# Optimization experiments

Hardware: AMD Instinct MI355X
Metric: run time of the kernel (lower is better)

## Reference

```python
import jax, jax.numpy as jnp
import numpy as np

N_NODES = 50000
N_EDGES = 800000
DIM = 128
N_LAYERS = 4
EPS = 1e-5  # BatchNorm1d default eps


def setup_inputs() -> dict:
    key = jax.random.key(0)
    k_x, k_e, k_w = jax.random.split(key, 3)
    x = jax.random.normal(k_x, (N_NODES, DIM), dtype=jnp.float32)
    edge_index = jax.random.randint(k_e, (2, N_EDGES), 0, N_NODES, dtype=jnp.int32)
    # stacked per-layer params (input_dim == hidden_dim == DIM)
    Ws = jax.random.normal(k_w, (N_LAYERS, DIM, DIM), dtype=jnp.float32) * (1.0 / np.sqrt(DIM))
    bs = jnp.zeros((N_LAYERS, DIM), jnp.float32)
    gammas = jnp.ones((N_LAYERS, DIM), jnp.float32)
    betas = jnp.zeros((N_LAYERS, DIM), jnp.float32)
    return {"x": x, "edge_index": edge_index, "Ws": Ws, "bs": bs,
            "gammas": gammas, "betas": betas}


def gcn_conv(x, W, b, src, dst, n):
    # PyG GCNConv: h = X W; out = D^{-1/2}(A+I)D^{-1/2} h + b
    h = x @ W                                       # [N, D]
    deg = jnp.zeros((n,), h.dtype).at[dst].add(1.0) + 1.0  # +1 self-loop
    dis = jax.lax.rsqrt(deg)                        # deg > 0 due to self-loops
    msg = h[src] * (dis[src] * dis[dst])[:, None]   # [E, D] gather + scale
    out = jnp.zeros_like(h).at[dst].add(msg)        # scatter-add aggregate
    out = out + h * (dis * dis)[:, None]            # self-loop term, norm = 1/deg
    return out + b


def batchnorm(z, gamma, beta):
    # BatchNorm1d training-mode math: batch mean, biased variance
    mu = z.mean(axis=0)
    var = z.var(axis=0)
    return (z - mu) * jax.lax.rsqrt(var + EPS) * gamma + beta


def reference(x, edge_index, Ws, bs, gammas, betas):
    src, dst = edge_index[0], edge_index[1]
    z = x
    for i in range(N_LAYERS):
        z = gcn_conv(z, Ws[i], bs[i], src, dst, z.shape[0])
        z = jax.nn.relu(z)
        z = batchnorm(z, gammas[i], betas[i])
        # Dropout: identity (eval mode / deterministic reference)
    return z
```

## Files before the change

### kernel.cpp

```cpp
#include <hip/hip_runtime.h>

#define N_NODES 50000
#define N_EDGES 800000
#define DIM 128
#define NLAYERS 4
#define BN_EPS 1e-5f
#define SCAN_BLOCKS 196
#define WSTRIDE 136

typedef __attribute__((ext_vector_type(8))) short short8;
typedef __attribute__((ext_vector_type(4))) float f32x4;

__device__ __forceinline__ float bf2f(unsigned short u){
    union { unsigned int i; float f; } x; x.i = ((unsigned int)u) << 16; return x.f;
}
__device__ __forceinline__ unsigned short f2bf(float f){
    union { float f; unsigned int i; } x; x.f = f;
    unsigned int lsb = (x.i >> 16) & 1u;
    unsigned int r = x.i + 0x7fffu + lsb;
    return (unsigned short)(r >> 16);
}

struct P4 { int2 a, b, c, d; };

__device__ __forceinline__ P4 loadP(const int2* __restrict__ ep, int base,
                                    int sub, int lim){
    P4 p;
    int i0 = base + sub, i1 = base + 4 + sub, i2 = base + 8 + sub, i3 = base + 12 + sub;
    p.a = (i0 < lim) ? ep[i0] : make_int2(0, 0);
    p.b = (i1 < lim) ? ep[i1] : make_int2(0, 0);
    p.c = (i2 < lim) ? ep[i2] : make_int2(0, 0);
    p.d = (i3 < lim) ? ep[i3] : make_int2(0, 0);
    return p;
}


__global__ __launch_bounds__(256) void k_zero(int* __restrict__ p, int n){
    int i = blockIdx.x * 256 + threadIdx.x;
    if (i < n) p[i] = 0;
}

__global__ __launch_bounds__(256) void k_count(const int* __restrict__ dst,
                                               int* __restrict__ degcnt){
    int e = blockIdx.x * 256 + threadIdx.x;
    if (e < N_EDGES) atomicAdd(&degcnt[dst[e]], 1);
}

__global__ __launch_bounds__(256) void k_scan1(const int* __restrict__ degcnt,
                                               int* __restrict__ rowptr,
                                               int* __restrict__ bsum,
                                               float* __restrict__ dis){
    __shared__ int tmp[256];
    int t = threadIdx.x;
    int i = blockIdx.x * 256 + t;
    int v = (i < N_NODES) ? degcnt[i] : 0;
    if (i < N_NODES) dis[i] = rsqrtf((float)v + 1.0f);
    tmp[t] = v;
    __syncthreads();
    #pragma unroll
    for (int off = 1; off < 256; off <<= 1){
        int u = (t >= off) ? tmp[t - off] : 0;
        __syncthreads();
        tmp[t] += u;
        __syncthreads();
    }
    if (i < N_NODES) rowptr[i] = tmp[t] - v;
    if (t == 255) bsum[blockIdx.x] = tmp[255];
}

__global__ __launch_bounds__(256) void k_scan2(int* __restrict__ bsum){
    __shared__ int tmp[256];
    int t = threadIdx.x;
    int v = (t < SCAN_BLOCKS) ? bsum[t] : 0;
    tmp[t] = v;
    __syncthreads();
    #pragma unroll
    for (int off = 1; off < 256; off <<= 1){
        int u = (t >= off) ? tmp[t - off] : 0;
        __syncthreads();
        tmp[t] += u;
        __syncthreads();
    }
    if (t < SCAN_BLOCKS) bsum[t] = tmp[t] - v;
}

__global__ __launch_bounds__(256) void k_scan3(const int* __restrict__ bsum,
                                               int* __restrict__ rowptr,
                                               int* __restrict__ wptr){
    int i = blockIdx.x * 256 + threadIdx.x;
    if (i < N_NODES){
        int r = rowptr[i] + bsum[blockIdx.x];
        rowptr[i] = r; wptr[i] = r;
    }
    if (i == 0) rowptr[N_NODES] = N_EDGES;
}

__global__ __launch_bounds__(256) void k_fill(const int* __restrict__ src,
                                              const int* __restrict__ dst,
                                              const float* __restrict__ dis,
                                              int* __restrict__ wptr,
                                              int2* __restrict__ epair){
    int e = blockIdx.x * 256 + threadIdx.x;
    if (e < N_EDGES){
        int s = src[e], d = dst[e];
        float w = dis[s] * dis[d];
        int p = atomicAdd(&wptr[d], 1);
        int2 pr; pr.x = s; pr.y = __float_as_int(w);
        epair[p] = pr;
    }
}

template<bool HAS>
__global__ __launch_bounds__(256) void k_wprep(const float* __restrict__ W,
                                               const float* __restrict__ scsh,
                                               unsigned short* __restrict__ wthi,
                                               unsigned short* __restrict__ wtlo,
                                               float* __restrict__ bias2){
    int tid = threadIdx.x;
    if (blockIdx.x < 64){
        int idx = blockIdx.x * 256 + tid;
        int c = idx >> 7, k = idx & 127;
        float v = W[k*DIM + c];
        if (HAS) v *= scsh[k];
        unsigned short hi = f2bf(v);
        float lo = v - bf2f(hi);
        wthi[c*DIM + k] = hi;
        wtlo[c*DIM + k] = f2bf(lo);
    } else {
        __shared__ float part[256];
        int c = tid >> 1, half = tid & 1;
        float acc = 0.f;
        if (HAS){
            int k0 = half * 64;
            #pragma unroll 4
            for (int k = k0; k < k0 + 64; k++)
                acc = fmaf(scsh[DIM + k], W[k*DIM + c], acc);
        }
        part[tid] = acc;
        __syncthreads();
        if (half == 0) bias2[c] = part[2*c] + part[2*c + 1];
    }
}


template<int MODE>
__global__ __launch_bounds__(256) void k_gemm(const void* __restrict__ zraw,
                                              const unsigned short* __restrict__ wthi,
                                              const unsigned short* __restrict__ wtlo,
                                              const float* __restrict__ bias2,
                                              unsigned short* __restrict__ hb){
    __shared__ short whi[DIM * WSTRIDE];
    __shared__ short wlo[DIM * WSTRIDE];
    int tid = threadIdx.x;

    {
        const uint4* gh = (const uint4*)wthi;
        const uint4* gl = (const uint4*)wtlo;
        #pragma unroll
        for (int it = 0; it < 8; it++){
            int ch = tid + 256*it;
            int c = ch >> 4, k8 = ch & 15;
            int off = c*WSTRIDE + k8*8;
            *(uint4*)&whi[off] = gh[ch];
            *(uint4*)&wlo[off] = gl[ch];
        }
    }
    __syncthreads();

    int lane = tid & 63;
    int wv   = tid >> 6;
    int m = lane & 15;
    int q = lane >> 4;
    int row0 = blockIdx.x * 64 + wv * 16;
    int arow = row0 + m;
    bool avalid = arow < N_NODES;

    f32x4 acc[8];
    #pragma unroll
    for (int t = 0; t < 8; t++) acc[t] = (f32x4){0.f, 0.f, 0.f, 0.f};

    #pragma unroll
    for (int g = 0; g < 4; g++){
        short8 a = {0,0,0,0,0,0,0,0};
        if (avalid){
            if (MODE == 0){
                const float* xp = (const float*)zraw + (size_t)arow*DIM + g*32 + q*8;
                float4 v0 = *(const float4*)xp;
                float4 v1 = *(const float4*)(xp + 4);
                a[0] = (short)f2bf(v0.x); a[1] = (short)f2bf(v0.y);
                a[2] = (short)f2bf(v0.z); a[3] = (short)f2bf(v0.w);
                a[4] = (short)f2bf(v1.x); a[5] = (short)f2bf(v1.y);
                a[6] = (short)f2bf(v1.z); a[7] = (short)f2bf(v1.w);
            } else {
                a = *(const short8*)((const unsigned short*)zraw
                      + (size_t)g*N_NODES*32 + (size_t)arow*32 + q*8);
            }
        }
        #pragma unroll
        for (int t = 0; t < 8; t++){
            int col = t*16 + m;
            int off = col*WSTRIDE + g*32 + q*8;
            short8 bh = *(const short8*)&whi[off];
            short8 bl = *(const short8*)&wlo[off];
            acc[t] = __builtin_amdgcn_mfma_f32_16x16x32_bf16(a, bh, acc[t], 0, 0, 0);
            acc[t] = __builtin_amdgcn_mfma_f32_16x16x32_bf16(a, bl, acc[t], 0, 0, 0);
        }
    }

    #pragma unroll
    for (int t = 0; t < 8; t++){
        int colg = t*16 + m;
        float bz = bias2[colg];
        size_t base = (size_t)(t >> 1)*N_NODES*32 + (t & 1)*16 + m;
        #pragma unroll
        for (int r = 0; r < 4; r++){
            int row = row0 + q*4 + r;
            if (row < N_NODES)
                hb[base + (size_t)row*32] = f2bf(acc[t][r] + bz);
        }
    }
}

__global__ __launch_bounds__(256) void k_agg(const unsigned short* __restrict__ h,
                                             const int* __restrict__ rowptr,
                                             const int2* __restrict__ epair,
                                             const float* __restrict__ dis,
                                             const float* __restrict__ bias,
                                             unsigned short* __restrict__ out,
                                             float* __restrict__ stats){
    int lane = threadIdx.x & 63;
    int w    = threadIdx.x >> 6;
    int g    = blockIdx.x & 3;
    int sub  = lane >> 4;
    int cp   = lane & 15;
    const ushort2* hg = (const ushort2*)(h + (size_t)g * N_NODES * 32);
    ushort2* og = (ushort2*)(out + (size_t)g * N_NODES * 32);
    float b0 = bias[g*32 + 2*cp], b1 = bias[g*32 + 2*cp + 1];
    float s0 = 0.f, s1 = 0.f, q0 = 0.f, q1 = 0.f;
    int bg = blockIdx.x >> 2;
    int nstride = (gridDim.x >> 2) * 4;

    int node = bg*4 + w;
    int ne0 = 0, ne1 = 0;
    ushort2 nhv; nhv.x = 0; nhv.y = 0;
    float ndi = 0.f;
    P4 nP = {{0,0},{0,0},{0,0},{0,0}};
    if (node < N_NODES){
        ne0 = rowptr[node];
        ne1 = rowptr[node + 1];
        nhv = hg[node*16 + cp];
        ndi = dis[node];
        nP  = loadP(epair, ne0, sub, ne1);
    }

    while (node < N_NODES){
        int e0 = ne0, e1 = ne1;
        ushort2 hv = nhv;
        float di = ndi;
        P4 P = nP;

        int nnext = node + nstride;
        if (nnext < N_NODES){
            ne0 = rowptr[nnext];
            ne1 = rowptr[nnext + 1];
            nhv = hg[nnext*16 + cp];
            ndi = dis[nnext];
        } else { ne0 = 0; ne1 = 0; }

        float pa0 = 0.f, pa1 = 0.f, pb0 = 0.f, pb1 = 0.f;
        float pc0 = 0.f, pc1 = 0.f, pd0 = 0.f, pd1 = 0.f;
        if (sub == 0){
            float dii = di * di;
            pa0 = bf2f(hv.x) * dii; pa1 = bf2f(hv.y) * dii;
        }

        int e = e0;
        while (e < e1){
            int en = e + 16;
            P4 Pn = {{0,0},{0,0},{0,0},{0,0}};
            if (en < e1) Pn = loadP(epair, en, sub, e1);
            ushort2 X0 = hg[P.a.x*16 + cp];
            ushort2 X1 = hg[P.b.x*16 + cp];
            ushort2 X2 = hg[P.c.x*16 + cp];
            ushort2 X3 = hg[P.d.x*16 + cp];
            float w0 = __int_as_float(P.a.y), w1 = __int_as_float(P.b.y);
            float w2 = __int_as_float(P.c.y), w3 = __int_as_float(P.d.y);
            pa0 = fmaf(bf2f(X0.x), w0, pa0); pa1 = fmaf(bf2f(X0.y), w0, pa1);
            pb0 = fmaf(bf2f(X1.x), w1, pb0); pb1 = fmaf(bf2f(X1.y), w1, pb1);
            pc0 = fmaf(bf2f(X2.x), w2, pc0); pc1 = fmaf(bf2f(X2.y), w2, pc1);
            pd0 = fmaf(bf2f(X3.x), w3, pd0); pd1 = fmaf(bf2f(X3.y), w3, pd1);
            P = Pn;
            e = en;
        }

        float r0 = (pa0 + pb0) + (pc0 + pd0);
        float r1 = (pa1 + pb1) + (pc1 + pd1);
        r0 += __shfl_xor(r0, 16); r1 += __shfl_xor(r1, 16);
        r0 += __shfl_xor(r0, 32); r1 += __shfl_xor(r1, 32);
        if (sub == 0){
            float a0 = fmaxf(r0 + b0, 0.f);
            float a1 = fmaxf(r1 + b1, 0.f);
            ushort2 ov; ov.x = f2bf(a0); ov.y = f2bf(a1);
            og[node*16 + cp] = ov;
            s0 += a0; s1 += a1; q0 += a0*a0; q1 += a1*a1;
        }

        if (nnext < N_NODES)
            nP = loadP(epair, ne0, sub, ne1);
        node = nnext;
    }

    __shared__ float red[4][16][4];
    if (sub == 0){
        red[w][cp][0] = s0; red[w][cp][1] = s1;
        red[w][cp][2] = q0; red[w][cp][3] = q1;
    }
    __syncthreads();
    if (w == 0 && sub == 0){
        #pragma unroll
        for (int ww = 1; ww < 4; ww++){
            s0 += red[ww][cp][0]; s1 += red[ww][cp][1];
            q0 += red[ww][cp][2]; q1 += red[ww][cp][3];
        }
        int c = g*32 + 2*cp;
        atomicAdd(&stats[c],         s0);
        atomicAdd(&stats[c + 1],     s1);
        atomicAdd(&stats[DIM + c],     q0);
        atomicAdd(&stats[DIM + c + 1], q1);
    }
}

__global__ void k_bnstat(const float* __restrict__ stats,
                         const float* __restrict__ gamma,
                         const float* __restrict__ beta,
                         float* __restrict__ scsh){
    int c = threadIdx.x;
    float mu  = stats[c] * (1.0f / N_NODES);
    float var = stats[DIM + c] * (1.0f / N_NODES) - mu * mu;
    float sc  = rsqrtf(var + BN_EPS) * gamma[c];
    scsh[c] = sc;
    scsh[DIM + c] = beta[c] - mu * sc;
}

__global__ __launch_bounds__(256) void k_bn(const uint4* __restrict__ in,
                                            const float* __restrict__ scsh,
                                            float4* __restrict__ outf){
    int i = blockIdx.x * 256 + threadIdx.x;
    if (i >= N_NODES * DIM / 8) return;
    int row = i >> 4;
    int c = (i * 8) & (DIM - 1);
    int gg = c >> 5, wi = c & 31;
    uint4 raw = in[gg*(N_NODES*4) + row*4 + (wi >> 3)];
    float4 sc0 = *(const float4*)&scsh[c];
    float4 sc1 = *(const float4*)&scsh[c + 4];
    float4 sh0 = *(const float4*)&scsh[DIM + c];
    float4 sh1 = *(const float4*)&scsh[DIM + c + 4];
    unsigned int u[4] = {raw.x, raw.y, raw.z, raw.w};
    float v[8];
    #pragma unroll
    for (int j = 0; j < 4; j++){
        v[2*j]   = bf2f((unsigned short)(u[j] & 0xffff));
        v[2*j+1] = bf2f((unsigned short)(u[j] >> 16));
    }
    float4 r0, r1;
    r0.x = fmaf(v[0], sc0.x, sh0.x);
    r0.y = fmaf(v[1], sc0.y, sh0.y);
    r0.z = fmaf(v[2], sc0.z, sh0.z);
    r0.w = fmaf(v[3], sc0.w, sh0.w);
    r1.x = fmaf(v[4], sc1.x, sh1.x);
    r1.y = fmaf(v[5], sc1.y, sh1.y);
    r1.z = fmaf(v[6], sc1.z, sh1.z);
    r1.w = fmaf(v[7], sc1.w, sh1.w);
    outf[2*i]   = r0;
    outf[2*i+1] = r1;
}


extern "C" void kernel_launch(void* const* d_in, const int* in_sizes, int n_in,
                              void* d_out, int out_size, void* d_ws, size_t ws_size,
                              hipStream_t stream){
    const float* x   = (const float*)d_in[0];
    const int*   src = (const int*)d_in[1];
    const int*   dst = src + N_EDGES;
    const float* Ws  = (const float*)d_in[2];
    const float* bs  = (const float*)d_in[3];
    const float* gs  = (const float*)d_in[4];
    const float* be  = (const float*)d_in[5];

    char* w = (char*)d_ws;
    int*   degcnt = (int*)(w);
    float* stats  = (float*)(w + 200000);
    float* scsh   = (float*)(w + 204096);
    float* dis    = (float*)(w + 208192);
    int*   rowptr = (int*)(w + 408192);
    int*   wptr   = (int*)(w + 608208);
    int*   bsum   = (int*)(w + 808208);
    float* bias2  = (float*)(w + 809232);
    unsigned short* wthi = (unsigned short*)(w + 809744);
    unsigned short* wtlo = (unsigned short*)(w + 842512);
    int2*  epair  = (int2*)(w + 875280);
    unsigned short* bufA = (unsigned short*)(w + 7275280);
    unsigned short* hb   = (unsigned short*)(w + 20075280);

    k_zero<<<(51024 + 255)/256, 256, 0, stream>>>(degcnt, 51024);
    k_count<<<3125, 256, 0, stream>>>(dst, degcnt);
    k_scan1<<<SCAN_BLOCKS, 256, 0, stream>>>(degcnt, rowptr, bsum, dis);
    k_scan2<<<1, 256, 0, stream>>>(bsum);
    k_scan3<<<SCAN_BLOCKS, 256, 0, stream>>>(bsum, rowptr, wptr);
    k_fill<<<3125, 256, 0, stream>>>(src, dst, dis, wptr, epair);

    for (int L = 0; L < NLAYERS; L++){
        const float* Wl = Ws + L*DIM*DIM;
        if (L == 0){
            k_wprep<false><<<65, 256, 0, stream>>>(Wl, nullptr, wthi, wtlo, bias2);
            k_gemm<0><<<(N_NODES + 63)/64, 256, 0, stream>>>(x, wthi, wtlo,
                                                             bias2, hb);
        } else {
            k_wprep<true><<<65, 256, 0, stream>>>(Wl, scsh + (L-1)*256,
                                                  wthi, wtlo, bias2);
            k_gemm<1><<<(N_NODES + 63)/64, 256, 0, stream>>>(bufA, wthi, wtlo,
                                                             bias2, hb);
        }
        k_agg<<<2048, 256, 0, stream>>>(hb, rowptr, epair, dis, bs + L*DIM,
                                        bufA, stats + L*256);
        k_bnstat<<<1, 128, 0, stream>>>(stats + L*256, gs + L*DIM, be + L*DIM,
                                        scsh + L*256);
    }
    k_bn<<<3125, 256, 0, stream>>>((const uint4*)bufA, scsh + 3*256,
                                   (float4*)d_out);
}
```

Measured before the change: 593.7 us.

## Fold BN stats into consumers, halve GEMM LDS footprint, add unmasked edge loads

Removes the per-layer single-block k_bnstat launch. The BN scale and shift are now recomputed from the raw stats inside k_wprep and k_bn, with k_bn caching them in shared memory. The GEMM stages the weight halves in two K-halves with a smaller LDS stride, which cuts shared memory per block and may allow more resident blocks, at the cost of an extra barrier. The edge-pair loader also gets an unmasked fast path for full 16-edge chunks. The trade-off is redundant rsqrt math in wprep, whose bias loop recomputes stats per k per thread.

```diff
diff --git a/kernel.cpp b/kernel.cpp
--- a/kernel.cpp
+++ b/kernel.cpp
@@ -6,7 +6,7 @@
 #define NLAYERS 4
 #define BN_EPS 1e-5f
 #define SCAN_BLOCKS 196
-#define WSTRIDE 136
+#define WS2 72
 
 typedef __attribute__((ext_vector_type(8))) short short8;
 typedef __attribute__((ext_vector_type(4))) float f32x4;
@@ -23,8 +23,8 @@
 
 struct P4 { int2 a, b, c, d; };
 
-__device__ __forceinline__ P4 loadP(const int2* __restrict__ ep, int base,
-                                    int sub, int lim){
+__device__ __forceinline__ P4 loadP_mask(const int2* __restrict__ ep, int base,
+                                         int sub, int lim){
     P4 p;
     int i0 = base + sub, i1 = base + 4 + sub, i2 = base + 8 + sub, i3 = base + 12 + sub;
     p.a = (i0 < lim) ? ep[i0] : make_int2(0, 0);
@@ -32,6 +32,20 @@
     p.c = (i2 < lim) ? ep[i2] : make_int2(0, 0);
     p.d = (i3 < lim) ? ep[i3] : make_int2(0, 0);
     return p;
+}
+__device__ __forceinline__ P4 loadP_full(const int2* __restrict__ ep, int base,
+                                         int sub){
+    P4 p;
+    p.a = ep[base + sub];
+    p.b = ep[base + 4 + sub];
+    p.c = ep[base + 8 + sub];
+    p.d = ep[base + 12 + sub];
+    return p;
+}
+__device__ __forceinline__ P4 loadP(const int2* __restrict__ ep, int base,
+                                    int sub, int lim){
+    if (lim - base >= 16) return loadP_full(ep, base, sub);
+    return loadP_mask(ep, base, sub, lim);
 }
 
 
@@ -112,7 +126,9 @@
 
 template<bool HAS>
 __global__ __launch_bounds__(256) void k_wprep(const float* __restrict__ W,
-                                               const float* __restrict__ scsh,
+                                               const float* __restrict__ stats,
+                                               const float* __restrict__ gamma,
+                                               const float* __restrict__ beta,
                                                unsigned short* __restrict__ wthi,
                                                unsigned short* __restrict__ wtlo,
                                                float* __restrict__ bias2){
@@ -121,7 +137,12 @@
         int idx = blockIdx.x * 256 + tid;
         int c = idx >> 7, k = idx & 127;
         float v = W[k*DIM + c];
-        if (HAS) v *= scsh[k];
+        if (HAS){
+            float mu  = stats[k] * (1.0f / N_NODES);
+            float var = stats[DIM + k] * (1.0f / N_NODES) - mu * mu;
+            float sc  = rsqrtf(var + BN_EPS) * gamma[k];
+            v *= sc;
+        }
         unsigned short hi = f2bf(v);
         float lo = v - bf2f(hi);
         wthi[c*DIM + k] = hi;
@@ -133,8 +154,13 @@
         if (HAS){
             int k0 = half * 64;
             #pragma unroll 4
-            for (int k = k0; k < k0 + 64; k++)
-                acc = fmaf(scsh[DIM + k], W[k*DIM + c], acc);
+            for (int k = k0; k < k0 + 64; k++){
+                float mu  = stats[k] * (1.0f / N_NODES);
+                float var = stats[DIM + k] * (1.0f / N_NODES) - mu * mu;
+                float sc  = rsqrtf(var + BN_EPS) * gamma[k];
+                float sh  = beta[k] - mu * sc;
+                acc = fmaf(sh, W[k*DIM + c], acc);
+            }
         }
         part[tid] = acc;
         __syncthreads();
@@ -149,23 +175,9 @@
                                               const unsigned short* __restrict__ wtlo,
                                               const float* __restrict__ bias2,
                                               unsigned short* __restrict__ hb){
-    __shared__ short whi[DIM * WSTRIDE];
-    __shared__ short wlo[DIM * WSTRIDE];
+    __shared__ short whi[DIM * WS2];
+    __shared__ short wlo[DIM * WS2];
     int tid = threadIdx.x;
-
-    {
-        const uint4* gh = (const uint4*)wthi;
-        const uint4* gl = (const uint4*)wtlo;
-        #pragma unroll
-        for (int it = 0; it < 8; it++){
-            int ch = tid + 256*it;
-            int c = ch >> 4, k8 = ch & 15;
-            int off = c*WSTRIDE + k8*8;
-            *(uint4*)&whi[off] = gh[ch];
-            *(uint4*)&wlo[off] = gl[ch];
-        }
-    }
-    __syncthreads();
 
     int lane = tid & 63;
     int wv   = tid >> 6;
@@ -179,32 +191,51 @@
     #pragma unroll
     for (int t = 0; t < 8; t++) acc[t] = (f32x4){0.f, 0.f, 0.f, 0.f};
 
-    #pragma unroll
-    for (int g = 0; g < 4; g++){
-        short8 a = {0,0,0,0,0,0,0,0};
-        if (avalid){
-            if (MODE == 0){
-                const float* xp = (const float*)zraw + (size_t)arow*DIM + g*32 + q*8;
-                float4 v0 = *(const float4*)xp;
-                float4 v1 = *(const float4*)(xp + 4);
-                a[0] = (short)f2bf(v0.x); a[1] = (short)f2bf(v0.y);
-                a[2] = (short)f2bf(v0.z); a[3] = (short)f2bf(v0.w);
-                a[4] = (short)f2bf(v1.x); a[5] = (short)f2bf(v1.y);
-                a[6] = (short)f2bf(v1.z); a[7] = (short)f2bf(v1.w);
-            } else {
-                a = *(const short8*)((const unsigned short*)zraw
-                      + (size_t)g*N_NODES*32 + (size_t)arow*32 + q*8);
+    const uint4* gh = (const uint4*)wthi;
+    const uint4* gl = (const uint4*)wtlo;
+
+    #pragma unroll
+    for (int half = 0; half < 2; half++){
+        #pragma unroll
+        for (int it = 0; it < 4; it++){
+            int ch = tid + 256*it;
+            int c = ch >> 3, k8 = ch & 7;
+            int off = c*WS2 + k8*8;
+            int srci = c*16 + half*8 + k8;
+            *(uint4*)&whi[off] = gh[srci];
+            *(uint4*)&wlo[off] = gl[srci];
+        }
+        __syncthreads();
+
+        #pragma unroll
+        for (int gl2 = 0; gl2 < 2; gl2++){
+            int gg = half*2 + gl2;
+            short8 a = {0,0,0,0,0,0,0,0};
+            if (avalid){
+                if (MODE == 0){
+                    const float* xp = (const float*)zraw + (size_t)arow*DIM + gg*32 + q*8;
+                    float4 v0 = *(const float4*)xp;
+                    float4 v1 = *(const float4*)(xp + 4);
+                    a[0] = (short)f2bf(v0.x); a[1] = (short)f2bf(v0.y);
+                    a[2] = (short)f2bf(v0.z); a[3] = (short)f2bf(v0.w);
+                    a[4] = (short)f2bf(v1.x); a[5] = (short)f2bf(v1.y);
+                    a[6] = (short)f2bf(v1.z); a[7] = (short)f2bf(v1.w);
+                } else {
+                    a = *(const short8*)((const unsigned short*)zraw
+                          + (size_t)gg*N_NODES*32 + (size_t)arow*32 + q*8);
+                }
             }
-        }
-        #pragma unroll
-        for (int t = 0; t < 8; t++){
-            int col = t*16 + m;
-            int off = col*WSTRIDE + g*32 + q*8;
-            short8 bh = *(const short8*)&whi[off];
-            short8 bl = *(const short8*)&wlo[off];
-            acc[t] = __builtin_amdgcn_mfma_f32_16x16x32_bf16(a, bh, acc[t], 0, 0, 0);
-            acc[t] = __builtin_amdgcn_mfma_f32_16x16x32_bf16(a, bl, acc[t], 0, 0, 0);
-        }
+            #pragma unroll
+            for (int t = 0; t < 8; t++){
+                int col = t*16 + m;
+                int off = col*WS2 + gl2*32 + q*8;
+                short8 bh = *(const short8*)&whi[off];
+                short8 bl = *(const short8*)&wlo[off];
+                acc[t] = __builtin_amdgcn_mfma_f32_16x16x32_bf16(a, bh, acc[t], 0, 0, 0);
+                acc[t] = __builtin_amdgcn_mfma_f32_16x16x32_bf16(a, bl, acc[t], 0, 0, 0);
+            }
+        }
+        if (half == 0) __syncthreads();
     }
 
     #pragma unroll
@@ -330,31 +361,28 @@
     }
 }
 
-__global__ void k_bnstat(const float* __restrict__ stats,
-                         const float* __restrict__ gamma,
-                         const float* __restrict__ beta,
-                         float* __restrict__ scsh){
-    int c = threadIdx.x;
-    float mu  = stats[c] * (1.0f / N_NODES);
-    float var = stats[DIM + c] * (1.0f / N_NODES) - mu * mu;
-    float sc  = rsqrtf(var + BN_EPS) * gamma[c];
-    scsh[c] = sc;
-    scsh[DIM + c] = beta[c] - mu * sc;
-}
-
 __global__ __launch_bounds__(256) void k_bn(const uint4* __restrict__ in,
-                                            const float* __restrict__ scsh,
+                                            const float* __restrict__ stats,
+                                            const float* __restrict__ gamma,
+                                            const float* __restrict__ beta,
                                             float4* __restrict__ outf){
-    int i = blockIdx.x * 256 + threadIdx.x;
+    __shared__ float scs[DIM], shs[DIM];
+    int tid = threadIdx.x;
+    if (tid < DIM){
+        float mu  = stats[tid] * (1.0f / N_NODES);
+        float var = stats[DIM + tid] * (1.0f / N_NODES) - mu * mu;
+        float sc  = rsqrtf(var + BN_EPS) * gamma[tid];
+        scs[tid] = sc;
+        shs[tid] = beta[tid] - mu * sc;
+    }
+    __syncthreads();
+
+    int i = blockIdx.x * 256 + tid;
     if (i >= N_NODES * DIM / 8) return;
     int row = i >> 4;
     int c = (i * 8) & (DIM - 1);
     int gg = c >> 5, wi = c & 31;
     uint4 raw = in[gg*(N_NODES*4) + row*4 + (wi >> 3)];
-    float4 sc0 = *(const float4*)&scsh[c];
-    float4 sc1 = *(const float4*)&scsh[c + 4];
-    float4 sh0 = *(const float4*)&scsh[DIM + c];
-    float4 sh1 = *(const float4*)&scsh[DIM + c + 4];
     unsigned int u[4] = {raw.x, raw.y, raw.z, raw.w};
     float v[8];
     #pragma unroll
@@ -363,14 +391,14 @@
         v[2*j+1] = bf2f((unsigned short)(u[j] >> 16));
     }
     float4 r0, r1;
-    r0.x = fmaf(v[0], sc0.x, sh0.x);
-    r0.y = fmaf(v[1], sc0.y, sh0.y);
-    r0.z = fmaf(v[2], sc0.z, sh0.z);
-    r0.w = fmaf(v[3], sc0.w, sh0.w);
-    r1.x = fmaf(v[4], sc1.x, sh1.x);
-    r1.y = fmaf(v[5], sc1.y, sh1.y);
-    r1.z = fmaf(v[6], sc1.z, sh1.z);
-    r1.w = fmaf(v[7], sc1.w, sh1.w);
+    r0.x = fmaf(v[0], scs[c+0], shs[c+0]);
+    r0.y = fmaf(v[1], scs[c+1], shs[c+1]);
+    r0.z = fmaf(v[2], scs[c+2], shs[c+2]);
+    r0.w = fmaf(v[3], scs[c+3], shs[c+3]);
+    r1.x = fmaf(v[4], scs[c+4], shs[c+4]);
+    r1.y = fmaf(v[5], scs[c+5], shs[c+5]);
+    r1.z = fmaf(v[6], scs[c+6], shs[c+6]);
+    r1.w = fmaf(v[7], scs[c+7], shs[c+7]);
     outf[2*i]   = r0;
     outf[2*i+1] = r1;
 }
@@ -390,7 +418,6 @@
     char* w = (char*)d_ws;
     int*   degcnt = (int*)(w);
     float* stats  = (float*)(w + 200000);
-    float* scsh   = (float*)(w + 204096);
     float* dis    = (float*)(w + 208192);
     int*   rowptr = (int*)(w + 408192);
     int*   wptr   = (int*)(w + 608208);
@@ -412,20 +439,20 @@
     for (int L = 0; L < NLAYERS; L++){
         const float* Wl = Ws + L*DIM*DIM;
         if (L == 0){
-            k_wprep<false><<<65, 256, 0, stream>>>(Wl, nullptr, wthi, wtlo, bias2);
+            k_wprep<false><<<65, 256, 0, stream>>>(Wl, nullptr, nullptr, nullptr,
+                                                   wthi, wtlo, bias2);
             k_gemm<0><<<(N_NODES + 63)/64, 256, 0, stream>>>(x, wthi, wtlo,
                                                              bias2, hb);
         } else {
-            k_wprep<true><<<65, 256, 0, stream>>>(Wl, scsh + (L-1)*256,
+            k_wprep<true><<<65, 256, 0, stream>>>(Wl, stats + (L-1)*256,
+                                                  gs + (L-1)*DIM, be + (L-1)*DIM,
                                                   wthi, wtlo, bias2);
             k_gemm<1><<<(N_NODES + 63)/64, 256, 0, stream>>>(bufA, wthi, wtlo,
                                                              bias2, hb);
         }
         k_agg<<<2048, 256, 0, stream>>>(hb, rowptr, epair, dis, bs + L*DIM,
                                         bufA, stats + L*256);
-        k_bnstat<<<1, 128, 0, stream>>>(stats + L*256, gs + L*DIM, be + L*DIM,
-                                        scsh + L*256);
-    }
-    k_bn<<<3125, 256, 0, stream>>>((const uint4*)bufA, scsh + 3*256,
-                                   (float4*)d_out);
-}
+    }
+    k_bn<<<3125, 256, 0, stream>>>((const uint4*)bufA, stats + 3*256,
+                                   gs + 3*DIM, be + 3*DIM, (float4*)d_out);
+}
```

Result: faster. 566.1 us (-4.6%).
